# Optimization experiments

Measured on AMD Instinct MI355X. Metric: run time of the kernel, lower is better.

The kernel has to match this reference:

```python
import jax, jax.numpy as jnp
import numpy as np

B, N, D, H, G = 4, 2048, 384, 8, 512
K = 8            # knn neighbors (hardcoded in get_graph_feature)
HID = 4 * D      # mlp_ratio = 4
FIN = 3 + G      # fuse_mlp in_features


def _ln(x, g, b, eps=1e-5):
    m = x.mean(-1, keepdims=True)
    v = ((x - m) ** 2).mean(-1, keepdims=True)
    return (x - m) * jax.lax.rsqrt(v + eps) * g + b


def _self_attn(x, qkv_w, pw, pb):
    b, n, c = x.shape
    hd = c // H
    qkv = (x @ qkv_w).reshape(b, n, 3, H, hd).transpose(2, 0, 3, 1, 4)
    q, k, v = qkv[0], qkv[1], qkv[2]                      # [b,h,n,hd]
    a = jax.nn.softmax(jnp.einsum('bhnd,bhmd->bhnm', q, k) * hd ** -0.5, -1)
    o = jnp.einsum('bhnm,bhmd->bhnd', a, v).transpose(0, 2, 1, 3).reshape(b, n, c)
    return o @ pw + pb


def _cross_attn(q, v, qw, kw, vw, pw, pb):
    b, n, c = q.shape
    nk = v.shape[1]
    hd = c // H
    qh = (q @ qw).reshape(b, n, H, hd).transpose(0, 2, 1, 3)
    kh = (v @ kw).reshape(b, nk, H, hd).transpose(0, 2, 1, 3)
    vh = (v @ vw).reshape(b, nk, H, hd).transpose(0, 2, 1, 3)
    a = jax.nn.softmax(jnp.einsum('bhnd,bhmd->bhnm', qh, kh) * hd ** -0.5, -1)
    o = jnp.einsum('bhnm,bhmd->bhnd', a, vh).transpose(0, 2, 1, 3).reshape(b, n, c)
    return o @ pw + pb


def _graph_feature(x, knn_index, x_q=None):
    b, n, c = x.shape
    nq = x_q.shape[1] if x_q is not None else n
    feat = x.reshape(b * n, c)[knn_index.reshape(-1)].reshape(b, K, nq, c)
    xq = (x_q if x_q is not None else x)[:, None, :, :]   # [b,1,nq,c]
    return jnp.concatenate([feat - xq, jnp.broadcast_to(xq, feat.shape)], -1)


def setup_inputs():
    key = jax.random.key(0)
    ks = iter(jax.random.split(key, 32))
    nrm = lambda shape: jax.random.normal(next(ks), shape, jnp.float32) * 0.02
    f32 = jnp.float32
    inp = {
        'q': jax.random.normal(next(ks), (B, D, N), f32),
        'in_pos': jax.random.normal(next(ks), (B, 3, N), f32),
        'guide_coding': jax.random.normal(next(ks), (B, G), f32),
        'norm1_g': jnp.ones((D,), f32), 'norm1_b': jnp.zeros((D,), f32),
        'qkv_w': nrm((D, 3 * D)),
        'sa_proj_w': nrm((D, D)), 'sa_proj_b': jnp.zeros((D,), f32),
        'normq_g': jnp.ones((D,), f32), 'normq_b': jnp.zeros((D,), f32),
        'fuse1_w': nrm((FIN, FIN)), 'fuse1_b': jnp.zeros((FIN,), f32),
        'fuse2_w': nrm((FIN, D)), 'fuse2_b': jnp.zeros((D,), f32),
        'normv_g': jnp.ones((D,), f32), 'normv_b': jnp.zeros((D,), f32),
        'ca_q_w': nrm((D, D)), 'ca_k_w': nrm((D, D)), 'ca_v_w': nrm((D, D)),
        'ca_proj_w': nrm((D, D)), 'ca_proj_b': jnp.zeros((D,), f32),
        'norm2_g': jnp.ones((D,), f32), 'norm2_b': jnp.zeros((D,), f32),
        'mlp1_w': nrm((D, HID)), 'mlp1_b': jnp.zeros((HID,), f32),
        'mlp2_w': nrm((HID, D)), 'mlp2_b': jnp.zeros((D,), f32),
        'knn_w': nrm((2 * D, D)), 'knn_b': jnp.zeros((D,), f32),
        'merge_w': nrm((2 * D, D)), 'merge_b': jnp.zeros((D,), f32),
        'knnx_w': nrm((2 * D, D)), 'knnx_b': jnp.zeros((D,), f32),
        'mergex_w': nrm((2 * D, D)), 'mergex_b': jnp.zeros((D,), f32),
        'self_knn_index': jax.random.randint(next(ks), (B, K, N), 0, B * N),
        'cross_knn_index': jax.random.randint(next(ks), (B, K, N), 0, B * N),
    }
    return inp


def reference(q, in_pos, guide_coding, norm1_g, norm1_b, qkv_w, sa_proj_w, sa_proj_b,
              normq_g, normq_b, fuse1_w, fuse1_b, fuse2_w, fuse2_b, normv_g, normv_b,
              ca_q_w, ca_k_w, ca_v_w, ca_proj_w, ca_proj_b, norm2_g, norm2_b,
              mlp1_w, mlp1_b, mlp2_w, mlp2_b, knn_w, knn_b, merge_w, merge_b,
              knnx_w, knnx_b, mergex_w, mergex_b, self_knn_index, cross_knn_index):
    npoints = in_pos.shape[2]
    q = q.transpose(0, 2, 1)                              # [B,N,D]
    norm_q = _ln(q, norm1_g, norm1_b)
    q_1 = _self_attn(norm_q, qkv_w, sa_proj_w, sa_proj_b)
    # build v from positions + broadcast guide coding
    gc = jnp.broadcast_to(guide_coding[:, :, None], (q.shape[0], G, npoints))
    v = jnp.concatenate([in_pos, gc], axis=1).transpose(0, 2, 1)  # [B,N,3+G]
    v = jax.nn.gelu(v @ fuse1_w + fuse1_b, approximate=False) @ fuse2_w + fuse2_b
    # self knn branch
    knn_f = _graph_feature(norm_q, self_knn_index)        # [B,K,N,2D]
    knn_f = jax.nn.leaky_relu(knn_f @ knn_w + knn_b, 0.2).max(axis=1)
    q_1 = jnp.concatenate([q_1, knn_f], -1) @ merge_w + merge_b
    q = q + q_1
    norm_q = _ln(q, normq_g, normq_b)
    norm_v = _ln(v, normv_g, normv_b)
    q_2 = _cross_attn(norm_q, norm_v, ca_q_w, ca_k_w, ca_v_w, ca_proj_w, ca_proj_b)
    # cross knn branch
    knn_f = _graph_feature(norm_v, cross_knn_index, norm_q)
    knn_f = jax.nn.leaky_relu(knn_f @ knnx_w + knnx_b, 0.2).max(axis=1)
    q_2 = jnp.concatenate([q_2, knn_f], -1) @ mergex_w + mergex_b
    q = q + q_2
    h = _ln(q, norm2_g, norm2_b)
    q = q + (jax.nn.gelu(h @ mlp1_w + mlp1_b, approximate=False) @ mlp2_w + mlp2_b)
    return q.transpose(0, 2, 1)                           # [B,D,N]
```

## Files before the change

kernel.cpp:

```cpp
#include <hip/hip_runtime.h>
#include <cstdint>
#include <cstddef>

#define B_ 4
#define N_ 2048
#define D_ 384
#define H_ 8
#define HD_ 48
#define G_ 512
#define K_ 8
#define HID_ 1536
#define FIN_ 515
#define FINP_ 520
#define M_ (B_*N_)
#define QSCALE 0.20823512f

typedef unsigned short u16;
typedef __attribute__((ext_vector_type(8))) short bf16x8;
typedef __attribute__((ext_vector_type(4))) float f32x4;

__device__ __forceinline__ u16 f2bf(float x){
  unsigned u = __builtin_bit_cast(unsigned, x);
  unsigned r = (u + 0x7fffu + ((u >> 16) & 1u)) >> 16;
  return (u16)r;
}
__device__ __forceinline__ float bf2f(u16 v){
  unsigned u = ((unsigned)v) << 16;
  return __builtin_bit_cast(float, u);
}
__device__ __forceinline__ float exp2_hw(float x){
  float r;
  asm("v_exp_f32 %0, %1" : "=v"(r) : "v"(x));
  return r;
}
__device__ __forceinline__ float gelu_f(float x){
  return 0.5f*x*(1.f + erff(x*0.70710678118654752f));
}

__global__ __launch_bounds__(256) void transpose_k(const float* __restrict__ in,
    float* __restrict__ out, int R, int C){
  __shared__ float tile[32][33];
  int b = blockIdx.z;
  int c0 = blockIdx.x<<5, r0 = blockIdx.y<<5;
  const float* ip = in + (size_t)b*R*C;
  float* op = out + (size_t)b*R*C;
  int tx = threadIdx.x, ty = threadIdx.y;
  #pragma unroll
  for (int i = ty; i < 32; i += 8)
    tile[i][tx] = ip[(size_t)(r0+i)*C + c0 + tx];
  __syncthreads();
  #pragma unroll
  for (int i = ty; i < 32; i += 8)
    op[(size_t)(c0+i)*R + r0 + tx] = tile[tx][i];
}

struct WJob { const float* src; u16* dst; int Kd, Nd, Kp, diff, nbx, blk0; };
struct WJobs { WJob j[16]; };

__global__ __launch_bounds__(256) void wtconv_all(WJobs J){
  int b = blockIdx.x, ji = 0;
  #pragma unroll
  for (int i=1;i<16;i++) if (b >= J.j[i].blk0) ji = i;
  WJob jb = J.j[ji];
  int local = b - jb.blk0;
  int bx = local % jb.nbx, by = local / jb.nbx;
  __shared__ float tile[32][33];
  int k0 = bx<<5, n0 = by<<5;
  int tx = threadIdx.x, ty = threadIdx.y;
  #pragma unroll
  for (int i = ty; i < 32; i += 8){
    int k = k0+i, n = n0+tx;
    float v = 0.f;
    if (k < jb.Kd && n < jb.Nd){
      v = jb.src[(size_t)k*jb.Nd + n];
      if (jb.diff) v = jb.src[(size_t)(k+jb.diff)*jb.Nd + n] - v;
    }
    tile[i][tx] = v;
  }
  __syncthreads();
  #pragma unroll
  for (int i = ty; i < 32; i += 8){
    int n = n0+i, k = k0+tx;
    if (n < jb.Nd && k < jb.Kp) jb.dst[(size_t)n*jb.Kp + k] = f2bf(tile[tx][i]);
  }
}

struct WP { const float *pw, *mwt, *pb, *mb2; u16* W; float* Bo; };
__global__ __launch_bounds__(256) void wprod_k(WP a, WP b){
  WP w = blockIdx.y ? b : a;
  int idx = blockIdx.x*256 + threadIdx.x;
  if (idx >= 385*384) return;
  int n = idx % 384, kk = idx / 384;
  float acc = 0.f;
  if (kk < 384){
    for (int j=0;j<384;j++) acc += w.pw[(size_t)kk*384+j] * w.mwt[(size_t)j*384+n];
    w.W[(size_t)n*768 + kk] = f2bf(acc);
  } else {
    for (int j=0;j<384;j++) acc += w.pb[j] * w.mwt[(size_t)j*384+n];
    w.Bo[n] = acc + w.mb2[n];
  }
}

__global__ __launch_bounds__(256) void biasfill_k(const float* __restrict__ knnb,
    const float* __restrict__ knnxb, float* __restrict__ bws){
  int i = blockIdx.x*256 + threadIdx.x;
  if (i < 2688){
    float v = 0.f;
    if (i >= 1536 && i < 1920) v = knnb[i-1536];
    else if (i >= 2304) v = knnxb[i-2304];
    bws[i] = v;
  }
}

__device__ __forceinline__ void ln_body(const float* xr, const float* g,
    const float* bta, u16* yr, float* sbuf, int t){
  float v0 = xr[t], v1 = xr[t+128], v2 = xr[t+256];
  float s = v0+v1+v2;
  #pragma unroll
  for (int off=32; off>0; off>>=1) s += __shfl_down(s, off, 64);
  int lane = t & 63, w = t >> 6;
  if (lane==0) sbuf[w] = s;
  __syncthreads();
  float mean = (sbuf[0]+sbuf[1]) * (1.f/(float)D_);
  float d0 = v0-mean, d1 = v1-mean, d2 = v2-mean;
  float s2 = d0*d0 + d1*d1 + d2*d2;
  #pragma unroll
  for (int off=32; off>0; off>>=1) s2 += __shfl_down(s2, off, 64);
  __syncthreads();
  if (lane==0) sbuf[w] = s2;
  __syncthreads();
  float inv = rsqrtf((sbuf[0]+sbuf[1])*(1.f/(float)D_) + 1e-5f);
  yr[t]     = f2bf(d0*inv*g[t]     + bta[t]);
  yr[t+128] = f2bf(d1*inv*g[t+128] + bta[t+128]);
  yr[t+256] = f2bf(d2*inv*g[t+256] + bta[t+256]);
}

__global__ __launch_bounds__(128) void ln_bf(const float* __restrict__ x,
    const float* __restrict__ g, const float* __restrict__ bta, u16* __restrict__ y){
  __shared__ float sbuf[2];
  int row = blockIdx.x;
  ln_body(x + (size_t)row*D_, g, bta, y + (size_t)row*D_, sbuf, threadIdx.x);
}

__global__ __launch_bounds__(128) void ln2_bf(const float* __restrict__ x0,
    const float* __restrict__ g0, const float* __restrict__ b0, u16* __restrict__ y0,
    const float* __restrict__ x1, const float* __restrict__ g1,
    const float* __restrict__ b1, u16* __restrict__ y1){
  __shared__ float sbuf[2];
  int row = blockIdx.x;
  if (row < M_)
    ln_body(x0 + (size_t)row*D_, g0, b0, y0 + (size_t)row*D_, sbuf, threadIdx.x);
  else {
    row -= M_;
    ln_body(x1 + (size_t)row*D_, g1, b1, y1 + (size_t)row*D_, sbuf, threadIdx.x);
  }
}

template<int ACT, int OUTBF, int ACCUM, int HASBIAS, int SCALEQ>
__global__ __launch_bounds__(512) void gemm8(const u16* __restrict__ A, int lda,
    const u16* __restrict__ Wt, int ldw, const float* __restrict__ bias,
    float* __restrict__ Cf, u16* __restrict__ Cb, int ldc, int Kd, int Nd, int Npad){
  __shared__ char Lmem[33280];
  u16* As = (u16*)Lmem;
  u16* Bs = As + 128*64;
  float* cred = (float*)Lmem;
  const int t = threadIdx.x;
  const int wv = t>>6, l = t&63;
  const int kg = wv>>2, wq = wv&3;
  const int wm = wq&1, wn = wq>>1;
  const int lr = l&15, ls = l>>4;
  const int bm = blockIdx.y<<7, bn = blockIdx.x<<6;
  f32x4 z4 = {0.f,0.f,0.f,0.f};
  f32x4 acc[4][2];
  #pragma unroll
  for (int mi=0;mi<4;mi++){ acc[mi][0]=z4; acc[mi][1]=z4; }
  const int Kup = (Kd+63)&~63;
  for (int k0=0; k0<Kup; k0+=64){
    #pragma unroll
    for (int i=0;i<2;i++){
      int g = t + (i<<9);
      int row = g>>3, slot = g&7;
      int kk = k0 + slot*8;
      float4 val = {0.f,0.f,0.f,0.f};
      if (kk < Kd) val = *reinterpret_cast<const float4*>(A + (size_t)(bm+row)*lda + kk);
      int ss = slot ^ (row&7);
      *reinterpret_cast<float4*>((char*)As + row*128 + ss*16) = val;
    }
    {
      int row = t>>3, slot = t&7;
      int kk = k0 + slot*8;
      int n = bn + row;
      float4 val = {0.f,0.f,0.f,0.f};
      if (n < Nd && kk < Kd) val = *reinterpret_cast<const float4*>(Wt + (size_t)n*ldw + kk);
      int ss = slot ^ (row&7);
      *reinterpret_cast<float4*>((char*)Bs + row*128 + ss*16) = val;
    }
    __syncthreads();
    bf16x8 af[4], bfr[2];
    #pragma unroll
    for (int mi=0;mi<4;mi++){
      int row = wm*64 + mi*16 + lr;
      int ss = (kg*4 + ls) ^ (row&7);
      af[mi] = *reinterpret_cast<bf16x8*>((char*)As + row*128 + ss*16);
    }
    #pragma unroll
    for (int ni=0;ni<2;ni++){
      int row = wn*32 + ni*16 + lr;
      int ss = (kg*4 + ls) ^ (row&7);
      bfr[ni] = *reinterpret_cast<bf16x8*>((char*)Bs + row*128 + ss*16);
    }
    #pragma unroll
    for (int mi=0;mi<4;mi++)
      #pragma unroll
      for (int ni=0;ni<2;ni++)
        acc[mi][ni] = __builtin_amdgcn_mfma_f32_16x16x32_bf16(af[mi], bfr[ni], acc[mi][ni], 0,0,0);
    __syncthreads();
  }
  if (kg == 1){
    #pragma unroll
    for (int mi=0;mi<4;mi++)
      #pragma unroll
      for (int ni=0;ni<2;ni++)
        #pragma unroll
        for (int r=0;r<4;r++){
          int row = wm*64 + mi*16 + ls*4 + r;
          int col = wn*32 + ni*16 + lr;
          cred[row*65 + col] = acc[mi][ni][r];
        }
  }
  __syncthreads();
  if (kg == 0){
    #pragma unroll
    for (int mi=0;mi<4;mi++){
      #pragma unroll
      for (int ni=0;ni<2;ni++){
        #pragma unroll
        for (int r=0;r<4;r++){
          int rl = wm*64 + mi*16 + ls*4 + r;
          int cl = wn*32 + ni*16 + lr;
          int row = bm + rl, col = bn + cl;
          float v = acc[mi][ni][r] + cred[rl*65 + cl];
          if (col < Nd){
            if (SCALEQ && col < 384) v *= QSCALE;
            if (HASBIAS) v += bias[col];
            if (ACT) v = gelu_f(v);
            if (OUTBF) Cb[(size_t)row*ldc + col] = f2bf(v);
            else if (ACCUM) Cf[(size_t)row*ldc + col] += v;
            else Cf[(size_t)row*ldc + col] = v;
          } else if (OUTBF && col < Npad){
            Cb[(size_t)row*ldc + col] = 0;
          }
        }
      }
    }
  }
}

__global__ __launch_bounds__(256) void vt_k(const u16* __restrict__ X, int ld,
                                            u16* __restrict__ Vt){
  __shared__ u16 tl[64][72];
  int bh = blockIdx.y, b = bh>>3, h = bh&7;
  int n0 = blockIdx.x<<6;
  #pragma unroll
  for (int i=0;i<2;i++){
    int g = threadIdx.x + (i<<8);
    if (g < 384){
      int r = g/6, c = (g - r*6)*8;
      *reinterpret_cast<float4*>(&tl[r][c]) =
        *reinterpret_cast<const float4*>(X + (size_t)(b*N_ + n0 + r)*ld + h*HD_ + c);
    }
  }
  __syncthreads();
  #pragma unroll
  for (int i=0;i<2;i++){
    int g = threadIdx.x + (i<<8);
    if (g < 384){
      int d = g % 48, sb = g / 48;
      u16 tmp[8];
      #pragma unroll
      for (int j=0;j<8;j++) tmp[j] = tl[sb*8+j][d];
      *reinterpret_cast<float4*>(Vt + ((size_t)(bh*HD_+d))*N_ + n0 + sb*8) =
        *reinterpret_cast<float4*>(tmp);
    }
  }
}

__global__ __launch_bounds__(256, 4) void attn_mfma(const u16* __restrict__ Qp, int ldq,
    const u16* __restrict__ Kp, int ldk, const u16* __restrict__ Vt,
    u16* __restrict__ O, int ldo){
  __shared__ u16 Kls[128*64];
  __shared__ u16 Vls[48*128];
  const int t = threadIdx.x, wv = t>>6, l = t&63;
  const int lr = l&15, ls = l>>4;
  const int bh = blockIdx.y, bb = bh>>3, h = bh&7;
  const int q0 = blockIdx.x<<6;
  bf16x8 zf = {0,0,0,0,0,0,0,0};
  f32x4 z4 = {0.f,0.f,0.f,0.f};
  const size_t rowQ = ((size_t)(bb*N_ + q0 + wv*16 + lr))*ldq + h*HD_;
  bf16x8 qa0 = *reinterpret_cast<const bf16x8*>(Qp + rowQ + 8*ls);
  bf16x8 qa1 = (ls < 2) ? *reinterpret_cast<const bf16x8*>(Qp + rowQ + 32 + 8*ls) : zf;
  f32x4 oacc[3] = {z4, z4, z4};
  float mrun = -1.0e30f, lrun = 0.f;
  for (int kt = 0; kt < N_/128; kt++){
    #pragma unroll
    for (int i=0;i<4;i++){
      int g = t + (i<<8);
      int key = g>>3, slot = g&7;
      float4 val = {0.f,0.f,0.f,0.f};
      if (slot < 6)
        val = *reinterpret_cast<const float4*>(Kp + (size_t)(bb*N_ + kt*128 + key)*ldk + h*HD_ + slot*8);
      *reinterpret_cast<float4*>((char*)Kls + key*128 + ((slot ^ (key&7))<<4)) = val;
    }
    #pragma unroll
    for (int i=0;i<3;i++){
      int g = t + (i<<8);
      int d = g>>4, m = g&15;
      float4 val = *reinterpret_cast<const float4*>(Vt + ((size_t)(bh*HD_+d))*N_ + kt*128 + m*8);
      float2 h0 = {val.x, val.y};
      float2 h1 = {val.z, val.w};
      int g4 = m*2;
      int sl0 = ((g4>>3)<<2) | (g4&3);
      int of0 = ((g4>>2)&1)<<3;
      *reinterpret_cast<float2*>((char*)Vls + d*256 + ((sl0 ^ (d&15))<<4) + of0) = h0;
      int g41 = g4 + 1;
      int sl1 = ((g41>>3)<<2) | (g41&3);
      int of1 = ((g41>>2)&1)<<3;
      *reinterpret_cast<float2*>((char*)Vls + d*256 + ((sl1 ^ (d&15))<<4) + of1) = h1;
    }
    __syncthreads();
    f32x4 S[8];
    #pragma unroll
    for (int sub=0; sub<8; sub++){
      int krow = sub*16 + lr;
      bf16x8 kb0 = *reinterpret_cast<bf16x8*>((char*)Kls + krow*128 + ((ls ^ (krow&7))<<4));
      bf16x8 kb1 = *reinterpret_cast<bf16x8*>((char*)Kls + krow*128 + (((4+ls) ^ (krow&7))<<4));
      f32x4 s = __builtin_amdgcn_mfma_f32_16x16x32_bf16(kb0, qa0, z4, 0,0,0);
      S[sub] = __builtin_amdgcn_mfma_f32_16x16x32_bf16(kb1, qa1, s, 0,0,0);
    }
    float tm = fmaxf(fmaxf(fmaxf(S[0][0],S[0][1]), fmaxf(S[0][2],S[0][3])),
                     fmaxf(fmaxf(S[1][0],S[1][1]), fmaxf(S[1][2],S[1][3])));
    #pragma unroll
    for (int sub=2;sub<8;sub++)
      tm = fmaxf(tm, fmaxf(fmaxf(S[sub][0],S[sub][1]), fmaxf(S[sub][2],S[sub][3])));
    if (__all(tm - mrun <= 10.f)){
      float ps = 0.f;
      #pragma unroll
      for (int sub=0;sub<8;sub++)
        #pragma unroll
        for (int r=0;r<4;r++){
          float p = exp2_hw(S[sub][r]-mrun);
          S[sub][r] = p; ps += p;
        }
      lrun += ps;
    } else {
      float mx = fmaxf(tm, __shfl_xor(tm, 16, 64));
      mx = fmaxf(mx, __shfl_xor(mx, 32, 64));
      float mnew = fmaxf(mrun, mx);
      float al = exp2_hw(mrun - mnew);
      mrun = mnew;
      float ps = 0.f;
      #pragma unroll
      for (int sub=0;sub<8;sub++)
        #pragma unroll
        for (int r=0;r<4;r++){
          float p = exp2_hw(S[sub][r]-mnew);
          S[sub][r] = p; ps += p;
        }
      lrun = lrun*al + ps;
      #pragma unroll
      for (int r=0;r<4;r++){
        float alq = __shfl(al, ls*4 + r, 64);
        oacc[0][r] *= alq; oacc[1][r] *= alq; oacc[2][r] *= alq;
      }
    }
    union PU { unsigned u[4]; bf16x8 v; };
    PU pa[4];
    #pragma unroll
    for (int kb=0;kb<4;kb++){
      asm("v_cvt_pk_bf16_f32 %0, %1, %2" : "=v"(pa[kb].u[0]) : "v"(S[2*kb][0]),   "v"(S[2*kb][1]));
      asm("v_cvt_pk_bf16_f32 %0, %1, %2" : "=v"(pa[kb].u[1]) : "v"(S[2*kb][2]),   "v"(S[2*kb][3]));
      asm("v_cvt_pk_bf16_f32 %0, %1, %2" : "=v"(pa[kb].u[2]) : "v"(S[2*kb+1][0]), "v"(S[2*kb+1][1]));
      asm("v_cvt_pk_bf16_f32 %0, %1, %2" : "=v"(pa[kb].u[3]) : "v"(S[2*kb+1][2]), "v"(S[2*kb+1][3]));
    }
    #pragma unroll
    for (int ni=0;ni<3;ni++){
      int d = ni*16 + lr;
      #pragma unroll
      for (int kb=0;kb<4;kb++){
        bf16x8 vb = *reinterpret_cast<bf16x8*>((char*)Vls + d*256 + ((((kb*4+ls) ^ (d&15)))<<4));
        oacc[ni] = __builtin_amdgcn_mfma_f32_16x16x32_bf16(pa[kb].v, vb, oacc[ni], 0,0,0);
      }
    }
    __syncthreads();
  }
  float sden = lrun;
  sden += __shfl_xor(sden, 16, 64);
  sden += __shfl_xor(sden, 32, 64);
  #pragma unroll
  for (int r=0;r<4;r++){
    float dq = __shfl(sden, ls*4 + r, 64);
    float inv = 1.f / dq;
    size_t orow = (size_t)(bb*N_ + q0 + wv*16 + ls*4 + r);
    #pragma unroll
    for (int ni=0;ni<3;ni++)
      O[orow*ldo + h*HD_ + ni*16 + lr] = f2bf(oacc[ni][r] * inv);
  }
}

__global__ __launch_bounds__(384) void gather_max_bf(const u16* __restrict__ P, int ldp,
    const u16* __restrict__ Q2, int ldq2, const int* __restrict__ idx,
    u16* __restrict__ out, int ldo){
  int m = blockIdx.x;
  int d = threadIdx.x;
  int b = m >> 11, n = m & (N_-1);
  float q2 = bf2f(Q2[(size_t)m*ldq2 + d]);
  float mx = -3.0e38f;
  #pragma unroll
  for (int k=0;k<K_;k++){
    int j = idx[((b<<3) + k)*N_ + n];
    float val = bf2f(P[(size_t)j*ldp + d]) + q2;
    val = (val >= 0.f) ? val : 0.2f*val;
    mx = fmaxf(mx, val);
  }
  out[(size_t)m*ldo + d] = f2bf(mx);
}

__global__ __launch_bounds__(256) void build_v(const float* __restrict__ pos,
    const float* __restrict__ gc, u16* __restrict__ v){
  int m = blockIdx.x;
  int b = m >> 11, n = m & (N_-1);
  for (int c = threadIdx.x; c < FINP_; c += 256){
    float val = 0.f;
    if (c < 3) val = pos[(b*3 + c)*N_ + n];
    else if (c < FIN_) val = gc[(b<<9) + (c-3)];
    v[(size_t)m*FINP_ + c] = f2bf(val);
  }
}

extern "C" void kernel_launch(void* const* d_in, const int* in_sizes, int n_in,
                              void* d_out, int out_size, void* d_ws, size_t ws_size,
                              hipStream_t stream){
  const float* q_in   = (const float*)d_in[0];
  const float* in_pos = (const float*)d_in[1];
  const float* guide  = (const float*)d_in[2];
  const float* n1g = (const float*)d_in[3];
  const float* n1b = (const float*)d_in[4];
  const float* qkv_w = (const float*)d_in[5];
  const float* sa_pw = (const float*)d_in[6];
  const float* sa_pb = (const float*)d_in[7];
  const float* nqg = (const float*)d_in[8];
  const float* nqb = (const float*)d_in[9];
  const float* f1w = (const float*)d_in[10];
  const float* f1b = (const float*)d_in[11];
  const float* f2w = (const float*)d_in[12];
  const float* f2b = (const float*)d_in[13];
  const float* nvg = (const float*)d_in[14];
  const float* nvb = (const float*)d_in[15];
  const float* caqw = (const float*)d_in[16];
  const float* cakw = (const float*)d_in[17];
  const float* cavw = (const float*)d_in[18];
  const float* capw = (const float*)d_in[19];
  const float* capb = (const float*)d_in[20];
  const float* n2g = (const float*)d_in[21];
  const float* n2b = (const float*)d_in[22];
  const float* m1w = (const float*)d_in[23];
  const float* m1b = (const float*)d_in[24];
  const float* m2w = (const float*)d_in[25];
  const float* m2b = (const float*)d_in[26];
  const float* knnw = (const float*)d_in[27];
  const float* knnb = (const float*)d_in[28];
  const float* mw = (const float*)d_in[29];
  const float* mb = (const float*)d_in[30];
  const float* knnxw = (const float*)d_in[31];
  const float* knnxb = (const float*)d_in[32];
  const float* mxw = (const float*)d_in[33];
  const float* mxb = (const float*)d_in[34];
  const int* sidx = (const int*)d_in[35];
  const int* cidx = (const int*)d_in[36];
  float* out = (float*)d_out;

  const size_t MD = (size_t)M_*D_;
  float* q_cur = (float*)d_ws;
  float* vbuf  = q_cur + MD;
  u16* R     = (u16*)(vbuf + MD);
  u16* nq_bf = R + (size_t)M_*1920;
  u16* nv_bf = nq_bf + MD;
  u16* cc    = nv_bf + MD;
  u16* vin   = cc + (size_t)M_*768;
  u16* e2    = vin + (size_t)M_*FINP_;
  u16* Vt    = e2 + (size_t)M_*FINP_;
  u16* wb    = Vt + (size_t)32*HD_*N_;
  u16* W1    = wb;  wb += (size_t)1920*384;
  u16* Wq    = wb;  wb += (size_t)768*384;
  u16* Wv    = wb;  wb += (size_t)1152*384;
  u16* Wfold = wb;  wb += (size_t)384*768;
  u16* Wfoldx= wb;  wb += (size_t)384*768;
  u16* f1T   = wb;  wb += (size_t)FIN_*FINP_;
  u16* f2T   = wb;  wb += (size_t)384*FINP_;
  u16* m1T   = wb;  wb += (size_t)1536*384;
  u16* m2T   = wb;  wb += (size_t)384*1536;
  if (((uintptr_t)wb & 3) != 0) wb++;
  float* bias_ws = (float*)wb;
  const size_t needed = (char*)(bias_ws + 3456) - (char*)d_ws;
  if (ws_size < needed) return;

  u16* X1 = R;
  u16* Xq = R;
  u16* Xv = R + (size_t)M_*768;
  u16* hid = R;

  dim3 tb32(32,8);
  transpose_k<<<dim3(N_/32, D_/32, B_), tb32, 0, stream>>>(q_in, q_cur, D_, N_);
  WJobs J;
  auto setj = [&](int i, const float* src, u16* dst, int Kd, int Nd, int Kp, int diff){
    J.j[i].src = src; J.j[i].dst = dst; J.j[i].Kd = Kd; J.j[i].Nd = Nd;
    J.j[i].Kp = Kp; J.j[i].diff = diff; J.j[i].nbx = (Kd+31)/32; J.j[i].blk0 = 0;
  };
  setj(0,  qkv_w, W1,                    384, 1152, 384, 0);
  setj(1,  knnw,  W1 + (size_t)1152*384, 384, 384, 384, 0);
  setj(2,  knnw,  W1 + (size_t)1536*384, 384, 384, 384, 384);
  setj(3,  caqw,  Wq,                    384, 384, 384, 0);
  setj(4,  knnxw, Wq + (size_t)384*384,  384, 384, 384, 384);
  setj(5,  cakw,  Wv,                    384, 384, 384, 0);
  setj(6,  cavw,  Wv + (size_t)384*384,  384, 384, 384, 0);
  setj(7,  knnxw, Wv + (size_t)768*384,  384, 384, 384, 0);
  setj(8,  mw  + (size_t)384*384, Wfold  + 384, 384, 384, 768, 0);
  setj(9,  mxw + (size_t)384*384, Wfoldx + 384, 384, 384, 768, 0);
  setj(10, f1w,   f1T, FIN_, FIN_, FINP_, 0);
  setj(11, f2w,   f2T, FIN_, 384, FINP_, 0);
  setj(12, m1w,   m1T, 384, 1536, 384, 0);
  setj(13, m2w,   m2T, 1536, 384, 1536, 0);
  int tot = 0;
  for (int i=0;i<14;i++){ J.j[i].blk0 = tot; tot += J.j[i].nbx * ((J.j[i].Nd+31)/32); }
  J.j[14] = J.j[13]; J.j[14].blk0 = 0x7fffffff; J.j[14].nbx = 1;
  J.j[15] = J.j[14];
  wtconv_all<<<tot, tb32, 0, stream>>>(J);
  WP wpa = { sa_pw, mw,  sa_pb, mb,  Wfold,  bias_ws + 2688 };
  WP wpb = { capw,  mxw, capb,  mxb, Wfoldx, bias_ws + 3072 };
  wprod_k<<<dim3(578, 2), 256, 0, stream>>>(wpa, wpb);
  biasfill_k<<<11, 256, 0, stream>>>(knnb, knnxb, bias_ws);
  ln_bf<<<M_, 128, 0, stream>>>(q_cur, n1g, n1b, nq_bf);
  gemm8<0,1,0,1,1><<<dim3(30, 64), 512, 0, stream>>>(nq_bf, 384, W1, 384, bias_ws, nullptr, X1, 1920, 384, 1920, 1920);
  vt_k<<<dim3(32, 32), 256, 0, stream>>>(X1 + 768, 1920, Vt);
  attn_mfma<<<dim3(32, 32), 256, 0, stream>>>(X1, 1920, X1 + 384, 1920, Vt, cc, 768);
  gather_max_bf<<<M_, 384, 0, stream>>>(X1 + 1152, 1920, X1 + 1536, 1920, sidx, cc + 384, 768);
  gemm8<0,0,1,1,0><<<dim3(6, 64), 512, 0, stream>>>(cc, 768, Wfold, 768, bias_ws + 2688, q_cur, nullptr, 384, 768, 384, 384);
  build_v<<<M_, 256, 0, stream>>>(in_pos, guide, vin);
  gemm8<1,1,0,1,0><<<dim3(9, 64), 512, 0, stream>>>(vin, FINP_, f1T, FINP_, f1b, nullptr, e2, FINP_, FIN_, FIN_, FINP_);
  gemm8<0,0,0,1,0><<<dim3(6, 64), 512, 0, stream>>>(e2, FINP_, f2T, FINP_, f2b, vbuf, nullptr, 384, FIN_, 384, 384);
  ln2_bf<<<2*M_, 128, 0, stream>>>(q_cur, nqg, nqb, nq_bf, vbuf, nvg, nvb, nv_bf);
  gemm8<0,1,0,1,1><<<dim3(12, 64), 512, 0, stream>>>(nq_bf, 384, Wq, 384, bias_ws + 1920, nullptr, Xq, 768, 384, 768, 768);
  gemm8<0,1,0,0,0><<<dim3(18, 64), 512, 0, stream>>>(nv_bf, 384, Wv, 384, nullptr, nullptr, Xv, 1152, 384, 1152, 1152);
  vt_k<<<dim3(32, 32), 256, 0, stream>>>(Xv + 384, 1152, Vt);
  attn_mfma<<<dim3(32, 32), 256, 0, stream>>>(Xq, 768, Xv, 1152, Vt, cc, 768);
  gather_max_bf<<<M_, 384, 0, stream>>>(Xv + 768, 1152, Xq + 384, 768, cidx, cc + 384, 768);
  gemm8<0,0,1,1,0><<<dim3(6, 64), 512, 0, stream>>>(cc, 768, Wfoldx, 768, bias_ws + 3072, q_cur, nullptr, 384, 768, 384, 384);
  ln_bf<<<M_, 128, 0, stream>>>(q_cur, n2g, n2b, nq_bf);
  gemm8<1,1,0,1,0><<<dim3(24, 64), 512, 0, stream>>>(nq_bf, 384, m1T, 384, m1b, nullptr, hid, 1536, 384, 1536, 1536);
  gemm8<0,0,1,1,0><<<dim3(6, 64), 512, 0, stream>>>(hid, 1536, m2T, 1536, m2b, q_cur, nullptr, 384, 1536, 384, 384);
  transpose_k<<<dim3(D_/32, N_/32, B_), tb32, 0, stream>>>(q_cur, out, N_, D_);
}
```

Before: 495.9 us.

## Prefetch next K/V tile into registers and simplify V LDS layout

The attention kernel now loads the next K and V tiles from global memory into registers right after the barrier, so the load latency overlaps with the current tile's MFMA work. Addresses and swizzle offsets are precomputed once outside the loop. V is stored to LDS as whole 16-byte chunks instead of split 8-byte pieces, and the read side is changed to gather two 8-byte halves per MFMA operand to match. This raises register pressure and doubles the number of LDS reads for V, which could reduce occupancy under the 256x4 launch bounds.

```diff
diff --git a/kernel.cpp b/kernel.cpp
--- a/kernel.cpp
+++ b/kernel.cpp
@@ -17,6 +17,7 @@
 
 typedef unsigned short u16;
 typedef __attribute__((ext_vector_type(8))) short bf16x8;
+typedef __attribute__((ext_vector_type(4))) short bf16x4;
 typedef __attribute__((ext_vector_type(4))) float f32x4;
 
 __device__ __forceinline__ u16 f2bf(float x){
@@ -296,38 +297,62 @@
   const int q0 = blockIdx.x<<6;
   bf16x8 zf = {0,0,0,0,0,0,0,0};
   f32x4 z4 = {0.f,0.f,0.f,0.f};
+  const float4 zero4 = {0.f,0.f,0.f,0.f};
   const size_t rowQ = ((size_t)(bb*N_ + q0 + wv*16 + lr))*ldq + h*HD_;
   bf16x8 qa0 = *reinterpret_cast<const bf16x8*>(Qp + rowQ + 8*ls);
   bf16x8 qa1 = (ls < 2) ? *reinterpret_cast<const bf16x8*>(Qp + rowQ + 32 + 8*ls) : zf;
   f32x4 oacc[3] = {z4, z4, z4};
   float mrun = -1.0e30f, lrun = 0.f;
+
+  int kofs[4]; const u16* kptr[4]; bool kval[4];
+  #pragma unroll
+  for (int i=0;i<4;i++){
+    int g = t + (i<<8);
+    int key = g>>3, slot = g&7;
+    kofs[i] = key*128 + ((slot ^ (key&7))<<4);
+    kval[i] = (slot < 6);
+    kptr[i] = Kp + (size_t)(bb*N_ + key)*ldk + h*HD_ + slot*8;
+  }
+  int vofs[3]; const u16* vptr[3];
+  #pragma unroll
+  for (int i=0;i<3;i++){
+    int g = t + (i<<8);
+    int d = g>>4, m = g&15;
+    vofs[i] = d*256 + ((m ^ (d&15))<<4);
+    vptr[i] = Vt + ((size_t)(bh*HD_+d))*N_ + m*8;
+  }
+  float4 kreg[4], vreg[3];
+  #pragma unroll
+  for (int i=0;i<4;i++){
+    kreg[i] = kval[i] ? *reinterpret_cast<const float4*>(kptr[i]) : zero4;
+    kptr[i] += (size_t)128*ldk;
+  }
+  #pragma unroll
+  for (int i=0;i<3;i++){
+    vreg[i] = *reinterpret_cast<const float4*>(vptr[i]);
+    vptr[i] += 128;
+  }
+
   for (int kt = 0; kt < N_/128; kt++){
     #pragma unroll
-    for (int i=0;i<4;i++){
-      int g = t + (i<<8);
-      int key = g>>3, slot = g&7;
-      float4 val = {0.f,0.f,0.f,0.f};
-      if (slot < 6)
-        val = *reinterpret_cast<const float4*>(Kp + (size_t)(bb*N_ + kt*128 + key)*ldk + h*HD_ + slot*8);
-      *reinterpret_cast<float4*>((char*)Kls + key*128 + ((slot ^ (key&7))<<4)) = val;
-    }
-    #pragma unroll
-    for (int i=0;i<3;i++){
-      int g = t + (i<<8);
-      int d = g>>4, m = g&15;
-      float4 val = *reinterpret_cast<const float4*>(Vt + ((size_t)(bh*HD_+d))*N_ + kt*128 + m*8);
-      float2 h0 = {val.x, val.y};
-      float2 h1 = {val.z, val.w};
-      int g4 = m*2;
-      int sl0 = ((g4>>3)<<2) | (g4&3);
-      int of0 = ((g4>>2)&1)<<3;
-      *reinterpret_cast<float2*>((char*)Vls + d*256 + ((sl0 ^ (d&15))<<4) + of0) = h0;
-      int g41 = g4 + 1;
-      int sl1 = ((g41>>3)<<2) | (g41&3);
-      int of1 = ((g41>>2)&1)<<3;
-      *reinterpret_cast<float2*>((char*)Vls + d*256 + ((sl1 ^ (d&15))<<4) + of1) = h1;
-    }
+    for (int i=0;i<4;i++)
+      *reinterpret_cast<float4*>((char*)Kls + kofs[i]) = kreg[i];
+    #pragma unroll
+    for (int i=0;i<3;i++)
+      *reinterpret_cast<float4*>((char*)Vls + vofs[i]) = vreg[i];
     __syncthreads();
+    if (kt+1 < N_/128){
+      #pragma unroll
+      for (int i=0;i<4;i++){
+        kreg[i] = kval[i] ? *reinterpret_cast<const float4*>(kptr[i]) : zero4;
+        kptr[i] += (size_t)128*ldk;
+      }
+      #pragma unroll
+      for (int i=0;i<3;i++){
+        vreg[i] = *reinterpret_cast<const float4*>(vptr[i]);
+        vptr[i] += 128;
+      }
+    }
     f32x4 S[8];
     #pragma unroll
     for (int sub=0; sub<8; sub++){
@@ -384,11 +409,15 @@
     }
     #pragma unroll
     for (int ni=0;ni<3;ni++){
-      int d = ni*16 + lr;
+      int dbase = (ni*16 + lr)*256 + ((ls&1)<<3);
       #pragma unroll
       for (int kb=0;kb<4;kb++){
-        bf16x8 vb = *reinterpret_cast<bf16x8*>((char*)Vls + d*256 + ((((kb*4+ls) ^ (d&15)))<<4));
-        oacc[ni] = __builtin_amdgcn_mfma_f32_16x16x32_bf16(pa[kb].v, vb, oacc[ni], 0,0,0);
+        union VU { bf16x4 h[2]; bf16x8 v; } vu;
+        int sA = ((kb*4 + (ls>>1)) ^ lr) << 4;
+        int sB = ((kb*4 + 2 + (ls>>1)) ^ lr) << 4;
+        vu.h[0] = *reinterpret_cast<bf16x4*>((char*)Vls + dbase + sA);
+        vu.h[1] = *reinterpret_cast<bf16x4*>((char*)Vls + dbase + sB);
+        oacc[ni] = __builtin_amdgcn_mfma_f32_16x16x32_bf16(pa[kb].v, vu.v, oacc[ni], 0,0,0);
       }
     }
     __syncthreads();
```

Measured after the change: 726.1 us. +46.4%, slower.

## Load attention K/V tiles directly to LDS with pre-swizzled V layout

Applied to the files above, without the earlier changes.

The V transpose kernel now writes V^T already in the swizzled per-tile layout that the attention kernel expects in shared memory. Both K and V tiles can then be copied with global_load_lds 16-byte direct-to-LDS loads instead of going through registers. Swizzled K offsets are precomputed once outside the loop. It also adds s_setprio around the MFMA sections and drops the occupancy hint from launch_bounds. K now loads all 8 slots, including padding columns 48-63 taken from the neighbouring head's data, which the zeroed qa1 lanes are meant to cancel. The risk is wrong results if that padding is not fully masked or the swizzle does not line up.

```diff
diff --git a/kernel.cpp b/kernel.cpp
--- a/kernel.cpp
+++ b/kernel.cpp
@@ -18,6 +18,10 @@
 typedef unsigned short u16;
 typedef __attribute__((ext_vector_type(8))) short bf16x8;
 typedef __attribute__((ext_vector_type(4))) float f32x4;
+
+#define GLOAD16(gp, lp) __builtin_amdgcn_global_load_lds( \
+    (const __attribute__((address_space(1))) void*)(gp), \
+    (__attribute__((address_space(3))) void*)(lp), 16, 0, 0)
 
 __device__ __forceinline__ u16 f2bf(float x){
   unsigned u = __builtin_bit_cast(unsigned, x);
@@ -276,16 +280,27 @@
     int g = threadIdx.x + (i<<8);
     if (g < 384){
       int d = g % 48, sb = g / 48;
-      u16 tmp[8];
-      #pragma unroll
-      for (int j=0;j<8;j++) tmp[j] = tl[sb*8+j][d];
-      *reinterpret_cast<float4*>(Vt + ((size_t)(bh*HD_+d))*N_ + n0 + sb*8) =
-        *reinterpret_cast<float4*>(tmp);
-    }
-  }
-}
-
-__global__ __launch_bounds__(256, 4) void attn_mfma(const u16* __restrict__ Qp, int ldq,
+      int hf = (n0>>6)&1;
+      int kt0 = n0 & ~127;
+      size_t rowb = ((size_t)(bh*HD_+d))*N_ + kt0;
+      int kA = hf*64 + sb*8;
+      ushort4 va, vb;
+      va.x = tl[sb*8+0][d]; va.y = tl[sb*8+1][d];
+      va.z = tl[sb*8+2][d]; va.w = tl[sb*8+3][d];
+      vb.x = tl[sb*8+4][d]; vb.y = tl[sb*8+5][d];
+      vb.z = tl[sb*8+6][d]; vb.w = tl[sb*8+7][d];
+      int uA = ((kA>>5)<<2) | ((kA>>2)&3);
+      int pA = (((uA ^ (d&15)))<<3) + (((kA>>4)&1)<<2);
+      int kB = kA + 4;
+      int uB = ((kB>>5)<<2) | ((kB>>2)&3);
+      int pB = (((uB ^ (d&15)))<<3) + (((kB>>4)&1)<<2);
+      *reinterpret_cast<ushort4*>(Vt + rowb + pA) = va;
+      *reinterpret_cast<ushort4*>(Vt + rowb + pB) = vb;
+    }
+  }
+}
+
+__global__ __launch_bounds__(256) void attn_mfma(const u16* __restrict__ Qp, int ldq,
     const u16* __restrict__ Kp, int ldk, const u16* __restrict__ Vt,
     u16* __restrict__ O, int ldo){
   __shared__ u16 Kls[128*64];
@@ -301,34 +316,36 @@
   bf16x8 qa1 = (ls < 2) ? *reinterpret_cast<const bf16x8*>(Qp + rowQ + 32 + 8*ls) : zf;
   f32x4 oacc[3] = {z4, z4, z4};
   float mrun = -1.0e30f, lrun = 0.f;
+
+  const u16* Kbase = Kp + (size_t)(bb*N_)*ldk + h*HD_;
+  const u16* Vbase = Vt + (size_t)bh*HD_*N_;
+  int kgo[4];
+  #pragma unroll
+  for (int i=0;i<4;i++){
+    int g = t + (i<<8);
+    int key = g>>3, s = g&7;
+    kgo[i] = key*ldk + ((s ^ (key&7))<<3);
+  }
+  int vgo[3];
+  #pragma unroll
+  for (int i=0;i<3;i++){
+    int g = t + (i<<8);
+    int d = g>>4, s = g&15;
+    vgo[i] = d*N_ + (s<<3);
+  }
+
   for (int kt = 0; kt < N_/128; kt++){
-    #pragma unroll
-    for (int i=0;i<4;i++){
-      int g = t + (i<<8);
-      int key = g>>3, slot = g&7;
-      float4 val = {0.f,0.f,0.f,0.f};
-      if (slot < 6)
-        val = *reinterpret_cast<const float4*>(Kp + (size_t)(bb*N_ + kt*128 + key)*ldk + h*HD_ + slot*8);
-      *reinterpret_cast<float4*>((char*)Kls + key*128 + ((slot ^ (key&7))<<4)) = val;
-    }
-    #pragma unroll
-    for (int i=0;i<3;i++){
-      int g = t + (i<<8);
-      int d = g>>4, m = g&15;
-      float4 val = *reinterpret_cast<const float4*>(Vt + ((size_t)(bh*HD_+d))*N_ + kt*128 + m*8);
-      float2 h0 = {val.x, val.y};
-      float2 h1 = {val.z, val.w};
-      int g4 = m*2;
-      int sl0 = ((g4>>3)<<2) | (g4&3);
-      int of0 = ((g4>>2)&1)<<3;
-      *reinterpret_cast<float2*>((char*)Vls + d*256 + ((sl0 ^ (d&15))<<4) + of0) = h0;
-      int g41 = g4 + 1;
-      int sl1 = ((g41>>3)<<2) | (g41&3);
-      int of1 = ((g41>>2)&1)<<3;
-      *reinterpret_cast<float2*>((char*)Vls + d*256 + ((sl1 ^ (d&15))<<4) + of1) = h1;
-    }
+    const u16* kp = Kbase + (size_t)kt*128*ldk;
+    #pragma unroll
+    for (int i=0;i<4;i++)
+      GLOAD16(kp + kgo[i], (char*)Kls + ((t + (i<<8))<<4));
+    const u16* vp = Vbase + kt*128;
+    #pragma unroll
+    for (int i=0;i<3;i++)
+      GLOAD16(vp + vgo[i], (char*)Vls + ((t + (i<<8))<<4));
     __syncthreads();
     f32x4 S[8];
+    __builtin_amdgcn_s_setprio(1);
     #pragma unroll
     for (int sub=0; sub<8; sub++){
       int krow = sub*16 + lr;
@@ -337,6 +354,7 @@
       f32x4 s = __builtin_amdgcn_mfma_f32_16x16x32_bf16(kb0, qa0, z4, 0,0,0);
       S[sub] = __builtin_amdgcn_mfma_f32_16x16x32_bf16(kb1, qa1, s, 0,0,0);
     }
+    __builtin_amdgcn_s_setprio(0);
     float tm = fmaxf(fmaxf(fmaxf(S[0][0],S[0][1]), fmaxf(S[0][2],S[0][3])),
                      fmaxf(fmaxf(S[1][0],S[1][1]), fmaxf(S[1][2],S[1][3])));
     #pragma unroll
@@ -382,6 +400,7 @@
       asm("v_cvt_pk_bf16_f32 %0, %1, %2" : "=v"(pa[kb].u[2]) : "v"(S[2*kb+1][0]), "v"(S[2*kb+1][1]));
       asm("v_cvt_pk_bf16_f32 %0, %1, %2" : "=v"(pa[kb].u[3]) : "v"(S[2*kb+1][2]), "v"(S[2*kb+1][3]));
     }
+    __builtin_amdgcn_s_setprio(1);
     #pragma unroll
     for (int ni=0;ni<3;ni++){
       int d = ni*16 + lr;
@@ -391,6 +410,7 @@
         oacc[ni] = __builtin_amdgcn_mfma_f32_16x16x32_bf16(pa[kb].v, vb, oacc[ni], 0,0,0);
       }
     }
+    __builtin_amdgcn_s_setprio(0);
     __syncthreads();
   }
   float sden = lrun;
```

Result: no change. 501.2 us (+1.1%).
